# Performance work log

Measured on AMD Instinct MI355X. Metric: run time of the kernel, lower is better.

Reference implementation:

```python
import jax, jax.numpy as jnp
import numpy as np

B, N, L = 1, 2048, 256
DX, DY, H = 1536, 768, 12
D = DX // H  # head_dim = 128
EPS_MOD = 1e-6   # modulated_rmsnorm eps
EPS_QK = 1e-5    # per-head RMSNorm eps


def setup_inputs() -> dict:
    key = jax.random.key(0)
    ks = jax.random.split(key, 16)
    def n(k, shape, s=1.0):
        return jax.random.normal(k, shape, dtype=jnp.float32) * s
    # rotary tables: (N, H, D//2), shared across heads
    pos = jnp.arange(N, dtype=jnp.float32)
    inv_freq = 1.0 / (10000.0 ** (jnp.arange(D // 2, dtype=jnp.float32) / (D // 2)))
    ang = pos[:, None] * inv_freq[None, :]                       # (N, D/2)
    rope_cos = jnp.broadcast_to(jnp.cos(ang)[:, None, :], (N, H, D // 2))
    rope_sin = jnp.broadcast_to(jnp.sin(ang)[:, None, :], (N, H, D // 2))
    return {
        "x": n(ks[0], (B, N, DX)),
        "y": n(ks[1], (B, L, DY)),
        "scale_x": n(ks[2], (B, DX), 0.1),
        "scale_y": n(ks[3], (B, DY), 0.1),
        "rope_cos": rope_cos,
        "rope_sin": rope_sin,
        "Wqkv_x": n(ks[4], (DX, 3 * DX), 0.02),
        "bqkv_x": jnp.zeros((3 * DX,), jnp.float32),
        "Wqkv_y": n(ks[5], (DY, 3 * DX), 0.02),
        "bqkv_y": jnp.zeros((3 * DX,), jnp.float32),
        "q_norm_x_w": jnp.ones((D,), jnp.float32),
        "k_norm_x_w": jnp.ones((D,), jnp.float32),
        "q_norm_y_w": jnp.ones((D,), jnp.float32),
        "k_norm_y_w": jnp.ones((D,), jnp.float32),
        "Wproj_x": n(ks[6], (DX, DX), 0.02),
        "bproj_x": jnp.zeros((DX,), jnp.float32),
        "Wproj_y": n(ks[7], (DX, DY), 0.02),
        "bproj_y": jnp.zeros((DY,), jnp.float32),
    }


def _rms(v, eps):
    return v * jax.lax.rsqrt(jnp.mean(v * v, axis=-1, keepdims=True) + eps)


def _rope(q, cos, sin):
    # q: (B, S, H, D); cos/sin: (S, H, D/2); even/odd interleaved rotation
    qe, qo = q[..., 0::2], q[..., 1::2]
    re = qe * cos - qo * sin
    ro = qe * sin + qo * cos
    return jnp.stack([re, ro], axis=-1).reshape(q.shape)


def reference(x, y, scale_x, scale_y, rope_cos, rope_sin,
              Wqkv_x, bqkv_x, Wqkv_y, bqkv_y,
              q_norm_x_w, k_norm_x_w, q_norm_y_w, k_norm_y_w,
              Wproj_x, bproj_x, Wproj_y, bproj_y):
    b, n, dx = x.shape
    _, l, _ = y.shape
    h, d = H, D
    # --- visual stream ---
    xm = _rms(x, EPS_MOD) * (1.0 + scale_x[:, None, :])          # modulated_rmsnorm
    qkv = (xm @ Wqkv_x + bqkv_x).reshape(b, n, 3, h, d)
    q_x, k_x, v_x = qkv[:, :, 0], qkv[:, :, 1], qkv[:, :, 2]
    q_x = _rope(_rms(q_x, EPS_QK) * q_norm_x_w, rope_cos, rope_sin)
    k_x = _rope(_rms(k_x, EPS_QK) * k_norm_x_w, rope_cos, rope_sin)
    # --- text stream ---
    ym = _rms(y, EPS_MOD) * (1.0 + scale_y[:, None, :])
    qkvy = (ym @ Wqkv_y + bqkv_y).reshape(b, l, 3, h, d)
    q_y, k_y, v_y = qkvy[:, :, 0], qkvy[:, :, 1], qkvy[:, :, 2]
    q_y = _rms(q_y, EPS_QK) * q_norm_y_w
    k_y = _rms(k_y, EPS_QK) * k_norm_y_w
    # --- joint attention over concatenated sequence (B, H, N+L, D) ---
    q = jnp.concatenate([q_x, q_y], axis=1).transpose(0, 2, 1, 3)
    k = jnp.concatenate([k_x, k_y], axis=1).transpose(0, 2, 1, 3)
    v = jnp.concatenate([v_x, v_y], axis=1).transpose(0, 2, 1, 3)
    scale = 1.0 / np.sqrt(d).astype(np.float32)
    attn = jax.nn.softmax(jnp.einsum('bhqd,bhkd->bhqk', q, k) * scale, axis=-1)
    out = jnp.einsum('bhqk,bhkd->bhqd', attn, v)
    out = out.transpose(0, 2, 1, 3).reshape(b, n + l, h * d)
    x_out = out[:, :n] @ Wproj_x + bproj_x
    y_out = out[:, n:] @ Wproj_y + bproj_y
    return (x_out, y_out)
```

## Files before the change

kernel.cpp:

```cpp
#include <hip/hip_runtime.h>

typedef unsigned short u16;
typedef __attribute__((ext_vector_type(8))) short short8;
typedef __attribute__((ext_vector_type(4))) short short4v;
typedef __attribute__((ext_vector_type(4))) float floatx4;

__device__ __forceinline__ u16 f2bf(float f) {
  return (u16)((__float_as_uint(f) + 0x8000u) >> 16);
}
__device__ __forceinline__ float bf2f(u16 v) {
  return __uint_as_float(((unsigned)v) << 16);
}
__device__ __forceinline__ unsigned pack_bf2(float a, float b) {
  const unsigned ua = __float_as_uint(a) + 0x8000u;
  const unsigned ub = __float_as_uint(b) + 0x8000u;
  return __builtin_amdgcn_perm(ub, ua, 0x07060302);
}

#define GLD16(g, l) __builtin_amdgcn_global_load_lds( \
    (const __attribute__((address_space(1))) void*)(g), \
    (__attribute__((address_space(3))) void*)(l), 16, 0, 0)

__global__ __launch_bounds__(256) void prep(const float* __restrict__ W0, u16* __restrict__ T0,
                                            const float* __restrict__ W1, u16* __restrict__ T1,
                                            const float* __restrict__ W2, u16* __restrict__ T2,
                                            const float* __restrict__ W3, u16* __restrict__ T3,
                                            const float* __restrict__ x, const float* __restrict__ scale_x,
                                            const float* __restrict__ y, const float* __restrict__ scale_y,
                                            u16* __restrict__ xm, u16* __restrict__ ym) {
  __shared__ float t[32][33];
  const int z = blockIdx.z;
  if (z < 4) {
    const float* in; u16* out; int K, N;
    switch (z) {
      case 0: in = W0; out = T0; K = 1536; N = 4608; break;
      case 1: in = W1; out = T1; K = 768;  N = 4608; break;
      case 2: in = W2; out = T2; K = 1536; N = 1536; break;
      default: in = W3; out = T3; K = 1536; N = 768; break;
    }
    const int n0 = blockIdx.x * 32, k0 = blockIdx.y * 32;
    if (n0 >= N || k0 >= K) return;
    const int tx = threadIdx.x, ty = threadIdx.y;
#pragma unroll
    for (int i = 0; i < 32; i += 8)
      t[ty + i][tx] = in[(size_t)(k0 + ty + i) * N + n0 + tx];
    __syncthreads();
#pragma unroll
    for (int i = 0; i < 32; i += 8)
      out[(size_t)(n0 + ty + i) * K + k0 + tx] = f2bf(t[tx][ty + i]);
  } else {
    const int row = blockIdx.y * 144 + blockIdx.x;
    if (row >= 2304) return;
    const int tid = threadIdx.y * 32 + threadIdx.x;
    const float* xr; const float* sc; u16* dst; int D;
    if (row < 2048) { D = 1536; xr = x + (size_t)row * D; sc = scale_x; dst = xm + (size_t)row * D; }
    else { D = 768; xr = y + (size_t)(row - 2048) * D; sc = scale_y; dst = ym + (size_t)(row - 2048) * D; }
    float ss = 0.f;
    for (int c = tid; c < D; c += 256) { float v = xr[c]; ss += v * v; }
    for (int off = 32; off > 0; off >>= 1) ss += __shfl_down(ss, off);
    __shared__ float red[4];
    if ((tid & 63) == 0) red[tid >> 6] = ss;
    __syncthreads();
    const float tot = red[0] + red[1] + red[2] + red[3];
    const float r = rsqrtf(tot / (float)D + 1e-6f);
    for (int c = tid; c < D; c += 256)
      dst[c] = f2bf(xr[c] * r * (1.0f + sc[c]));
  }
}

template <bool BOUT>
__global__ __launch_bounds__(256) void gemm2(const u16* __restrict__ A0, const u16* __restrict__ BT0,
                                             const float* __restrict__ bias0, void* __restrict__ C0,
                                             int M0, int N0, int K0,
                                             const u16* __restrict__ A1, const u16* __restrict__ BT1,
                                             const float* __restrict__ bias1, void* __restrict__ C1,
                                             int M1, int N1, int K1) {
  const u16 *A, *BT; const float* bias; void* Cout; int M, N, K;
  if (blockIdx.z == 0) { A = A0; BT = BT0; bias = bias0; Cout = C0; M = M0; N = N0; K = K0; }
  else { A = A1; BT = BT1; bias = bias1; Cout = C1; M = M1; N = N1; K = K1; }
  const int bm = blockIdx.y * 128, bn = blockIdx.x * 128;
  if (bm >= M || bn >= N) return;

  __shared__ __align__(16) u16 As[128 * 32];
  __shared__ __align__(16) u16 Bs[128 * 32];
  const int tid = threadIdx.x;
  const int lane = tid & 63, wave = tid >> 6;
  const int wm = (wave & 1) * 64, wn = (wave >> 1) * 64;
  const int row16 = lane & 15, quad = lane >> 4;

  floatx4 acc[4][4] = {};
  const int r0 = lane >> 2, c4 = (lane & 3) * 8;
  const u16* Ag0 = A + (size_t)(bm + wave * 16 + r0) * K + c4;
  const u16* Ag1 = A + (size_t)(bm + (wave + 4) * 16 + r0) * K + c4;
  const u16* Bg0 = BT + (size_t)(bn + wave * 16 + r0) * K + c4;
  const u16* Bg1 = BT + (size_t)(bn + (wave + 4) * 16 + r0) * K + c4;
  u16* As0 = As + wave * 512; u16* As1 = As + (wave + 4) * 512;
  u16* Bs0 = Bs + wave * 512; u16* Bs1 = Bs + (wave + 4) * 512;

  for (int k0 = 0; k0 < K; k0 += 32) {
    GLD16(Ag0 + k0, As0);
    GLD16(Ag1 + k0, As1);
    GLD16(Bg0 + k0, Bs0);
    GLD16(Bg1 + k0, Bs1);
    __syncthreads();
    short8 af[4], bf[4];
#pragma unroll
    for (int i = 0; i < 4; i++) {
      af[i] = *(const short8*)&As[(wm + i * 16 + row16) * 32 + quad * 8];
      bf[i] = *(const short8*)&Bs[(wn + i * 16 + row16) * 32 + quad * 8];
    }
#pragma unroll
    for (int mi = 0; mi < 4; mi++)
#pragma unroll
      for (int ni = 0; ni < 4; ni++)
        acc[mi][ni] = __builtin_amdgcn_mfma_f32_16x16x32_bf16(af[mi], bf[ni], acc[mi][ni], 0, 0, 0);
    __syncthreads();
  }
#pragma unroll
  for (int mi = 0; mi < 4; mi++) {
#pragma unroll
    for (int ni = 0; ni < 4; ni++) {
      const int col = bn + wn + ni * 16 + row16;
      const float b = bias[col];
      const int row0 = bm + wm + mi * 16 + quad * 4;
#pragma unroll
      for (int r = 0; r < 4; r++) {
        const float v = acc[mi][ni][r] + b;
        if constexpr (BOUT)
          ((u16*)Cout)[(size_t)(row0 + r) * N + col] = f2bf(v);
        else
          ((float*)Cout)[(size_t)(row0 + r) * N + col] = v;
      }
    }
  }
}

__global__ __launch_bounds__(128) void qkv_post(const u16* __restrict__ qkvx,
                                                const u16* __restrict__ qkvy,
                                                const float* __restrict__ qnwx, const float* __restrict__ knwx,
                                                const float* __restrict__ qnwy, const float* __restrict__ knwy,
                                                const float* __restrict__ rcos, const float* __restrict__ rsin,
                                                u16* __restrict__ Q, u16* __restrict__ Kb, u16* __restrict__ V) {
  const int s = blockIdx.x, h = blockIdx.y, d = threadIdx.x;
  const bool isx = s < 2048;
  const u16* base = isx ? (qkvx + (size_t)s * 4608) : (qkvy + (size_t)(s - 2048) * 4608);
  const float q = bf2f(base[h * 128 + d]);
  const float k = bf2f(base[1536 + h * 128 + d]);
  const u16 v = base[3072 + h * 128 + d];
  __shared__ float redq[2], redk[2];
  float sq = q * q, sk = k * k;
  for (int off = 32; off > 0; off >>= 1) { sq += __shfl_down(sq, off); sk += __shfl_down(sk, off); }
  const int lane = threadIdx.x & 63, w = threadIdx.x >> 6;
  if (lane == 0) { redq[w] = sq; redk[w] = sk; }
  __syncthreads();
  const float rq = rsqrtf((redq[0] + redq[1]) * (1.f / 128.f) + 1e-5f);
  const float rk = rsqrtf((redk[0] + redk[1]) * (1.f / 128.f) + 1e-5f);
  float qn = q * rq * (isx ? qnwx[d] : qnwy[d]);
  float kn = k * rk * (isx ? knwx[d] : knwy[d]);
  if (isx) {
    const int i = d >> 1;
    const float c = rcos[((size_t)s * 12 + h) * 64 + i];
    const float sn = rsin[((size_t)s * 12 + h) * 64 + i];
    const float qo = __shfl_xor(qn, 1);
    const float ko = __shfl_xor(kn, 1);
    qn = (d & 1) ? (qo * sn + qn * c) : (qn * c - qo * sn);
    kn = (d & 1) ? (ko * sn + kn * c) : (kn * c - ko * sn);
  }
  qn *= 0.12751737942f;
  const size_t o = ((size_t)h * 2304 + s) * 128 + d;
  Q[o] = f2bf(qn);
  Kb[o] = f2bf(kn);
  V[o] = v;
}

__global__ __launch_bounds__(256) void vtrans(const u16* __restrict__ V, u16* __restrict__ Vt) {
  __shared__ u16 t[32][33];
  const int h = blockIdx.x, st = blockIdx.y * 32, dt = blockIdx.z * 32;
  const u16* Vh = V + (size_t)h * 2304 * 128;
  u16* Vth = Vt + (size_t)h * 128 * 2304;
  const int tx = threadIdx.x, ty = threadIdx.y;
#pragma unroll
  for (int i = 0; i < 32; i += 8)
    t[ty + i][tx] = Vh[(size_t)(st + ty + i) * 128 + dt + tx];
  __syncthreads();
#pragma unroll
  for (int i = 0; i < 32; i += 8)
    Vth[(size_t)(dt + ty + i) * 2304 + st + tx] = t[tx][ty + i];
}

__global__ __launch_bounds__(256, 4) void attn(const u16* __restrict__ Q, const u16* __restrict__ Kb,
                                               const u16* __restrict__ Vt,
                                               u16* __restrict__ Opart,
                                               float* __restrict__ Mp, float* __restrict__ Lp) {
  const int h = blockIdx.y, split = blockIdx.z;
  const int q0 = blockIdx.x * 64;
  const int tid = threadIdx.x, lane = tid & 63, wave = tid >> 6;
  const int row16 = lane & 15, quad = lane >> 4;
  const u16* Qh = Q + (size_t)h * 2304 * 128;
  const u16* Kh = Kb + (size_t)h * 2304 * 128;
  const u16* Vh = Vt + (size_t)h * 128 * 2304;

  __shared__ __align__(16) u16 Ks[64 * 128];
  __shared__ __align__(16) u16 Vs[128 * 64];
  __shared__ __align__(16) u16 Ps[4][16 * 64];

  short8 qf[4];
  {
    const u16* qrow = Qh + (size_t)(q0 + wave * 16 + row16) * 128;
#pragma unroll
    for (int kk = 0; kk < 4; kk++) qf[kk] = *(const short8*)(qrow + kk * 32 + quad * 8);
  }
  floatx4 oacc[8] = {};
  float m_i = -1e30f, l_i = 0.f;

  int krow[4], kcol[4], vrow[4], vcol[4];
#pragma unroll
  for (int i = 0; i < 4; i++) {
    const int j = i * 4 + wave;
    krow[i] = j * 4 + (lane >> 4);
    kcol[i] = ((lane & 15) ^ (krow[i] & 7)) * 8;
    vrow[i] = j * 8 + (lane >> 3);
    vcol[i] = ((lane & 7) ^ (vrow[i] & 7)) * 8;
  }
  const int sw = row16 & 7;
  const int kbeg = split * 576, kend = kbeg + 576;

  for (int kt = kbeg; kt < kend; kt += 64) {
    __syncthreads();
#pragma unroll
    for (int i = 0; i < 4; i++) {
      GLD16(Kh + (size_t)(kt + krow[i]) * 128 + kcol[i], Ks + (i * 4 + wave) * 512);
      GLD16(Vh + (size_t)vrow[i] * 2304 + kt + vcol[i], Vs + (i * 4 + wave) * 512);
    }
    __syncthreads();

    floatx4 sacc[4] = {};
#pragma unroll
    for (int mk = 0; mk < 4; mk++) {
#pragma unroll
      for (int kk = 0; kk < 4; kk++) {
        const int c = (4 * kk + quad) ^ sw;
        const short8 kfrag = *(const short8*)&Ks[(mk * 16 + row16) * 128 + c * 8];
        sacc[mk] = __builtin_amdgcn_mfma_f32_16x16x32_bf16(kfrag, qf[kk], sacc[mk], 0, 0, 0);
      }
    }
    float mx = sacc[0][0];
#pragma unroll
    for (int mk = 0; mk < 4; mk++)
#pragma unroll
      for (int r = 0; r < 4; r++) mx = fmaxf(mx, sacc[mk][r]);
    mx = fmaxf(mx, __shfl_xor(mx, 16));
    mx = fmaxf(mx, __shfl_xor(mx, 32));
    const float mnew = fmaxf(m_i, mx);
    if (__any(mnew > m_i)) {
      const float alpha = exp2f(m_i - mnew);
      m_i = mnew;
      const float a0 = __shfl(alpha, quad * 4 + 0);
      const float a1 = __shfl(alpha, quad * 4 + 1);
      const float a2 = __shfl(alpha, quad * 4 + 2);
      const float a3 = __shfl(alpha, quad * 4 + 3);
#pragma unroll
      for (int nd = 0; nd < 8; nd++) {
        oacc[nd][0] *= a0; oacc[nd][1] *= a1; oacc[nd][2] *= a2; oacc[nd][3] *= a3;
      }
      l_i *= alpha;
    }
    float s = 0.f;
#pragma unroll
    for (int mk = 0; mk < 4; mk++) {
#pragma unroll
      for (int r = 0; r < 4; r++) {
        const float p = exp2f(sacc[mk][r] - m_i);
        sacc[mk][r] = p;
        s += p;
      }
    }
    s += __shfl_xor(s, 16);
    s += __shfl_xor(s, 32);
    l_i += s;

#pragma unroll
    for (int mk = 0; mk < 4; mk++) {
      const int subp = (4 * mk + quad) ^ (sw << 1);
      uint2 pk;
      pk.x = pack_bf2(sacc[mk][0], sacc[mk][1]);
      pk.y = pack_bf2(sacc[mk][2], sacc[mk][3]);
      *(uint2*)&Ps[wave][row16 * 64 + subp * 4] = pk;
    }
    const int pc0 = quad ^ sw, pc1 = (4 + quad) ^ sw;
    const short8 pf0 = *(const short8*)&Ps[wave][row16 * 64 + pc0 * 8];
    const short8 pf1 = *(const short8*)&Ps[wave][row16 * 64 + pc1 * 8];
#pragma unroll
    for (int nd = 0; nd < 8; nd++) {
      const short8 vf0 = *(const short8*)&Vs[(nd * 16 + row16) * 64 + pc0 * 8];
      const short8 vf1 = *(const short8*)&Vs[(nd * 16 + row16) * 64 + pc1 * 8];
      oacc[nd] = __builtin_amdgcn_mfma_f32_16x16x32_bf16(pf0, vf0, oacc[nd], 0, 0, 0);
      oacc[nd] = __builtin_amdgcn_mfma_f32_16x16x32_bf16(pf1, vf1, oacc[nd], 0, 0, 0);
    }
  }
  const size_t base = (size_t)(split * 12 + h) * 2304 + q0 + wave * 16;
#pragma unroll
  for (int nd = 0; nd < 8; nd++)
#pragma unroll
    for (int r = 0; r < 4; r++)
      Opart[(base + quad * 4 + r) * 128 + nd * 16 + row16] = f2bf(oacc[nd][r]);
  if (lane < 16) { Mp[base + lane] = m_i; Lp[base + lane] = l_i; }
}

__global__ __launch_bounds__(256) void attn_combine(const u16* __restrict__ Opart,
                                                    const float* __restrict__ Mp,
                                                    const float* __restrict__ Lp,
                                                    u16* __restrict__ attnout) {
  const int idx = blockIdx.x * 256 + threadIdx.x;
  const int dd = (idx & 31) * 4;
  const int hq = idx >> 5;
  const int h = hq % 12, q = hq / 12;
  size_t b[4]; float ms[4], ls[4];
  float m = -1e30f;
#pragma unroll
  for (int s = 0; s < 4; s++) {
    b[s] = (size_t)(s * 12 + h) * 2304 + q;
    ms[s] = Mp[b[s]]; ls[s] = Lp[b[s]];
    m = fmaxf(m, ms[s]);
  }
  float w[4], denom = 0.f;
#pragma unroll
  for (int s = 0; s < 4; s++) { w[s] = exp2f(ms[s] - m); denom += ls[s] * w[s]; }
  const float inv = 1.0f / denom;
  float ox = 0.f, oy = 0.f, oz = 0.f, ow = 0.f;
#pragma unroll
  for (int s = 0; s < 4; s++) {
    const short4v o = *(const short4v*)&Opart[b[s] * 128 + dd];
    ox += bf2f((u16)o[0]) * w[s]; oy += bf2f((u16)o[1]) * w[s];
    oz += bf2f((u16)o[2]) * w[s]; ow += bf2f((u16)o[3]) * w[s];
  }
  short4v out;
  out[0] = (short)f2bf(ox * inv);
  out[1] = (short)f2bf(oy * inv);
  out[2] = (short)f2bf(oz * inv);
  out[3] = (short)f2bf(ow * inv);
  *(short4v*)&attnout[(size_t)idx * 4] = out;
}

extern "C" void kernel_launch(void* const* d_in, const int* in_sizes, int n_in,
                              void* d_out, int out_size, void* d_ws, size_t ws_size,
                              hipStream_t stream) {
  const float* x        = (const float*)d_in[0];
  const float* y        = (const float*)d_in[1];
  const float* scale_x  = (const float*)d_in[2];
  const float* scale_y  = (const float*)d_in[3];
  const float* rope_cos = (const float*)d_in[4];
  const float* rope_sin = (const float*)d_in[5];
  const float* Wqkv_x   = (const float*)d_in[6];
  const float* bqkv_x   = (const float*)d_in[7];
  const float* Wqkv_y   = (const float*)d_in[8];
  const float* bqkv_y   = (const float*)d_in[9];
  const float* qnwx     = (const float*)d_in[10];
  const float* knwx     = (const float*)d_in[11];
  const float* qnwy     = (const float*)d_in[12];
  const float* knwy     = (const float*)d_in[13];
  const float* Wproj_x  = (const float*)d_in[14];
  const float* bproj_x  = (const float*)d_in[15];
  const float* Wproj_y  = (const float*)d_in[16];
  const float* bproj_y  = (const float*)d_in[17];
  float* out = (float*)d_out;

  char* ws = (char*)d_ws;
  size_t off = 0;
  auto take = [&](size_t bytes) { char* p = ws + off; off += (bytes + 255) & ~(size_t)255; return p; };
  u16* WqkvxT  = (u16*)take((size_t)4608 * 1536 * 2);
  u16* WqkvyT  = (u16*)take((size_t)4608 * 768 * 2);
  u16* WprojxT = (u16*)take((size_t)1536 * 1536 * 2);
  u16* WprojyT = (u16*)take((size_t)768 * 1536 * 2);
  u16* xm      = (u16*)take((size_t)2048 * 1536 * 2);
  u16* ym      = (u16*)take((size_t)256 * 768 * 2);
  u16* qkvx    = (u16*)take((size_t)2048 * 4608 * 2);
  u16* qkvy    = (u16*)take((size_t)256 * 4608 * 2);
  u16* Qb      = (u16*)take((size_t)12 * 2304 * 128 * 2);
  u16* Kb      = (u16*)take((size_t)12 * 2304 * 128 * 2);
  u16* Vb      = (u16*)take((size_t)12 * 2304 * 128 * 2);
  u16* Vt      = (u16*)take((size_t)12 * 128 * 2304 * 2);
  u16* attnout = (u16*)take((size_t)2304 * 1536 * 2);
  u16* Opart   = (u16*)take((size_t)4 * 12 * 2304 * 128 * 2);
  float* Mp    = (float*)take((size_t)4 * 12 * 2304 * 4);
  float* Lp    = (float*)take((size_t)4 * 12 * 2304 * 4);

  prep<<<dim3(144, 48, 5), dim3(32, 8), 0, stream>>>(Wqkv_x, WqkvxT, Wqkv_y, WqkvyT,
                                                     Wproj_x, WprojxT, Wproj_y, WprojyT,
                                                     x, scale_x, y, scale_y, xm, ym);

  gemm2<true><<<dim3(36, 16, 2), 256, 0, stream>>>(xm, WqkvxT, bqkv_x, qkvx, 2048, 4608, 1536,
                                                   ym, WqkvyT, bqkv_y, qkvy, 256, 4608, 768);

  qkv_post<<<dim3(2304, 12), 128, 0, stream>>>(qkvx, qkvy, qnwx, knwx, qnwy, knwy,
                                               rope_cos, rope_sin, Qb, Kb, Vb);
  vtrans<<<dim3(12, 2304 / 32, 128 / 32), dim3(32, 8), 0, stream>>>(Vb, Vt);

  attn<<<dim3(2304 / 64, 12, 4), 256, 0, stream>>>(Qb, Kb, Vt, Opart, Mp, Lp);
  attn_combine<<<(2304 * 1536 / 4) / 256, 256, 0, stream>>>(Opart, Mp, Lp, attnout);

  gemm2<false><<<dim3(12, 16, 2), 256, 0, stream>>>(attnout, WprojxT, bproj_x, out, 2048, 1536, 1536,
                                                    attnout + (size_t)2048 * 1536, WprojyT, bproj_y,
                                                    out + (size_t)2048 * 1536, 256, 768, 1536);
  (void)in_sizes; (void)n_in; (void)out_size; (void)ws_size;
}
```

Measured before the change: 327.7 us.

## Fuse V transpose into qkv_post and double query rows per attention wave

qkv_post now handles 32 tokens per block with vectorized 16-element loads. It writes V directly in transposed layout through a shared-memory tile, so the separate vtrans kernel and the intermediate V buffer are gone. The attention kernel now processes 32 query rows per wave (128 per block), reusing each K/V LDS fragment for two MFMA groups, and switches to 6 KV splits with a vectorized 8-wide combine. The intent is to cut global traffic and K/V reloads per query, at the cost of higher register pressure (launch bounds lowered to 3 blocks per CU) and more partial outputs to combine.

```diff
diff --git a/kernel.cpp b/kernel.cpp
--- a/kernel.cpp
+++ b/kernel.cpp
@@ -135,65 +135,93 @@
   }
 }
 
-__global__ __launch_bounds__(128) void qkv_post(const u16* __restrict__ qkvx,
+__global__ __launch_bounds__(256) void qkv_post(const u16* __restrict__ qkvx,
                                                 const u16* __restrict__ qkvy,
                                                 const float* __restrict__ qnwx, const float* __restrict__ knwx,
                                                 const float* __restrict__ qnwy, const float* __restrict__ knwy,
                                                 const float* __restrict__ rcos, const float* __restrict__ rsin,
-                                                u16* __restrict__ Q, u16* __restrict__ Kb, u16* __restrict__ V) {
-  const int s = blockIdx.x, h = blockIdx.y, d = threadIdx.x;
-  const bool isx = s < 2048;
+                                                u16* __restrict__ Q, u16* __restrict__ Kb, u16* __restrict__ Vt) {
+  const int s0 = blockIdx.x * 32, h = blockIdx.y;
+  const int tid = threadIdx.x;
+  const int r = tid >> 3, j = tid & 7, d0 = j * 16;
+  const int s = s0 + r;
+  const bool isx = s0 < 2048;
   const u16* base = isx ? (qkvx + (size_t)s * 4608) : (qkvy + (size_t)(s - 2048) * 4608);
-  const float q = bf2f(base[h * 128 + d]);
-  const float k = bf2f(base[1536 + h * 128 + d]);
-  const u16 v = base[3072 + h * 128 + d];
-  __shared__ float redq[2], redk[2];
-  float sq = q * q, sk = k * k;
-  for (int off = 32; off > 0; off >>= 1) { sq += __shfl_down(sq, off); sk += __shfl_down(sk, off); }
-  const int lane = threadIdx.x & 63, w = threadIdx.x >> 6;
-  if (lane == 0) { redq[w] = sq; redk[w] = sk; }
+
+  __shared__ __align__(16) u16 Vtile[128][40];
+
+  short8 q8a = *(const short8*)(base + h * 128 + d0);
+  short8 q8b = *(const short8*)(base + h * 128 + d0 + 8);
+  short8 k8a = *(const short8*)(base + 1536 + h * 128 + d0);
+  short8 k8b = *(const short8*)(base + 1536 + h * 128 + d0 + 8);
+  short8 v8a = *(const short8*)(base + 3072 + h * 128 + d0);
+  short8 v8b = *(const short8*)(base + 3072 + h * 128 + d0 + 8);
+
+  float qv[16], kv[16];
+  float sq = 0.f, sk = 0.f;
+#pragma unroll
+  for (int i = 0; i < 8; i++) {
+    qv[i] = bf2f((u16)q8a[i]); qv[8 + i] = bf2f((u16)q8b[i]);
+    kv[i] = bf2f((u16)k8a[i]); kv[8 + i] = bf2f((u16)k8b[i]);
+  }
+#pragma unroll
+  for (int i = 0; i < 16; i++) { sq += qv[i] * qv[i]; sk += kv[i] * kv[i]; }
+  sq += __shfl_xor(sq, 1); sq += __shfl_xor(sq, 2); sq += __shfl_xor(sq, 4);
+  sk += __shfl_xor(sk, 1); sk += __shfl_xor(sk, 2); sk += __shfl_xor(sk, 4);
+  const float rq = rsqrtf(sq * (1.f / 128.f) + 1e-5f);
+  const float rk = rsqrtf(sk * (1.f / 128.f) + 1e-5f);
+
+  const float* qw = isx ? qnwx : qnwy;
+  const float* kw = isx ? knwx : knwy;
+#pragma unroll
+  for (int i = 0; i < 16; i++) {
+    qv[i] *= rq * qw[d0 + i];
+    kv[i] *= rk * kw[d0 + i];
+  }
+  if (isx) {
+    const float* cp = rcos + ((size_t)s * 12 + h) * 64 + d0 / 2;
+    const float* sp = rsin + ((size_t)s * 12 + h) * 64 + d0 / 2;
+#pragma unroll
+    for (int i = 0; i < 16; i += 2) {
+      const float c = cp[i / 2], sn = sp[i / 2];
+      const float qe = qv[i], qo = qv[i + 1];
+      const float ke = kv[i], ko = kv[i + 1];
+      qv[i] = qe * c - qo * sn; qv[i + 1] = qe * sn + qo * c;
+      kv[i] = ke * c - ko * sn; kv[i + 1] = ke * sn + ko * c;
+    }
+  }
+  short8 qo8[2], ko8[2];
+#pragma unroll
+  for (int half = 0; half < 2; half++)
+#pragma unroll
+    for (int i = 0; i < 8; i++) {
+      qo8[half][i] = (short)f2bf(qv[half * 8 + i] * 0.12751737942f);
+      ko8[half][i] = (short)f2bf(kv[half * 8 + i]);
+    }
+  const size_t o = ((size_t)h * 2304 + s) * 128 + d0;
+  *(short8*)(Q + o) = qo8[0];  *(short8*)(Q + o + 8) = qo8[1];
+  *(short8*)(Kb + o) = ko8[0]; *(short8*)(Kb + o + 8) = ko8[1];
+
+#pragma unroll
+  for (int i = 0; i < 8; i++) {
+    Vtile[d0 + i][r] = (u16)v8a[i];
+    Vtile[d0 + 8 + i][r] = (u16)v8b[i];
+  }
   __syncthreads();
-  const float rq = rsqrtf((redq[0] + redq[1]) * (1.f / 128.f) + 1e-5f);
-  const float rk = rsqrtf((redk[0] + redk[1]) * (1.f / 128.f) + 1e-5f);
-  float qn = q * rq * (isx ? qnwx[d] : qnwy[d]);
-  float kn = k * rk * (isx ? knwx[d] : knwy[d]);
-  if (isx) {
-    const int i = d >> 1;
-    const float c = rcos[((size_t)s * 12 + h) * 64 + i];
-    const float sn = rsin[((size_t)s * 12 + h) * 64 + i];
-    const float qo = __shfl_xor(qn, 1);
-    const float ko = __shfl_xor(kn, 1);
-    qn = (d & 1) ? (qo * sn + qn * c) : (qn * c - qo * sn);
-    kn = (d & 1) ? (ko * sn + kn * c) : (kn * c - ko * sn);
-  }
-  qn *= 0.12751737942f;
-  const size_t o = ((size_t)h * 2304 + s) * 128 + d;
-  Q[o] = f2bf(qn);
-  Kb[o] = f2bf(kn);
-  V[o] = v;
-}
-
-__global__ __launch_bounds__(256) void vtrans(const u16* __restrict__ V, u16* __restrict__ Vt) {
-  __shared__ u16 t[32][33];
-  const int h = blockIdx.x, st = blockIdx.y * 32, dt = blockIdx.z * 32;
-  const u16* Vh = V + (size_t)h * 2304 * 128;
-  u16* Vth = Vt + (size_t)h * 128 * 2304;
-  const int tx = threadIdx.x, ty = threadIdx.y;
-#pragma unroll
-  for (int i = 0; i < 32; i += 8)
-    t[ty + i][tx] = Vh[(size_t)(st + ty + i) * 128 + dt + tx];
-  __syncthreads();
-#pragma unroll
-  for (int i = 0; i < 32; i += 8)
-    Vth[(size_t)(dt + ty + i) * 2304 + st + tx] = t[tx][ty + i];
-}
-
-__global__ __launch_bounds__(256, 4) void attn(const u16* __restrict__ Q, const u16* __restrict__ Kb,
+  const int d = tid >> 1, sh = (tid & 1) * 16;
+  short8 va = *(const short8*)&Vtile[d][sh];
+  short8 vb = *(const short8*)&Vtile[d][sh + 8];
+  u16* vdst = Vt + ((size_t)h * 128 + d) * 2304 + s0 + sh;
+  *(short8*)vdst = va;
+  *(short8*)(vdst + 8) = vb;
+}
+
+__global__ __launch_bounds__(256, 3) void attn(const u16* __restrict__ Q, const u16* __restrict__ Kb,
                                                const u16* __restrict__ Vt,
                                                u16* __restrict__ Opart,
                                                float* __restrict__ Mp, float* __restrict__ Lp) {
   const int h = blockIdx.y, split = blockIdx.z;
-  const int q0 = blockIdx.x * 64;
+  const int q0 = blockIdx.x * 128;
   const int tid = threadIdx.x, lane = tid & 63, wave = tid >> 6;
   const int row16 = lane & 15, quad = lane >> 4;
   const u16* Qh = Q + (size_t)h * 2304 * 128;
@@ -202,28 +230,29 @@
 
   __shared__ __align__(16) u16 Ks[64 * 128];
   __shared__ __align__(16) u16 Vs[128 * 64];
-  __shared__ __align__(16) u16 Ps[4][16 * 64];
-
-  short8 qf[4];
-  {
-    const u16* qrow = Qh + (size_t)(q0 + wave * 16 + row16) * 128;
-#pragma unroll
-    for (int kk = 0; kk < 4; kk++) qf[kk] = *(const short8*)(qrow + kk * 32 + quad * 8);
-  }
-  floatx4 oacc[8] = {};
-  float m_i = -1e30f, l_i = 0.f;
+  __shared__ __align__(16) u16 Ps[4][32 * 64];
+
+  short8 qf[2][4];
+#pragma unroll
+  for (int g = 0; g < 2; g++) {
+    const u16* qrow = Qh + (size_t)(q0 + wave * 32 + g * 16 + row16) * 128;
+#pragma unroll
+    for (int kk = 0; kk < 4; kk++) qf[g][kk] = *(const short8*)(qrow + kk * 32 + quad * 8);
+  }
+  floatx4 oacc[8][2] = {};
+  float m_i[2] = {-1e30f, -1e30f}, l_i[2] = {0.f, 0.f};
 
   int krow[4], kcol[4], vrow[4], vcol[4];
 #pragma unroll
   for (int i = 0; i < 4; i++) {
-    const int j = i * 4 + wave;
-    krow[i] = j * 4 + (lane >> 4);
+    const int jj = i * 4 + wave;
+    krow[i] = jj * 4 + (lane >> 4);
     kcol[i] = ((lane & 15) ^ (krow[i] & 7)) * 8;
-    vrow[i] = j * 8 + (lane >> 3);
+    vrow[i] = jj * 8 + (lane >> 3);
     vcol[i] = ((lane & 7) ^ (vrow[i] & 7)) * 8;
   }
   const int sw = row16 & 7;
-  const int kbeg = split * 576, kend = kbeg + 576;
+  const int kbeg = split * 384, kend = kbeg + 384;
 
   for (int kt = kbeg; kt < kend; kt += 64) {
     __syncthreads();
@@ -234,77 +263,104 @@
     }
     __syncthreads();
 
-    floatx4 sacc[4] = {};
+    floatx4 sacc[4][2] = {};
 #pragma unroll
     for (int mk = 0; mk < 4; mk++) {
 #pragma unroll
       for (int kk = 0; kk < 4; kk++) {
         const int c = (4 * kk + quad) ^ sw;
         const short8 kfrag = *(const short8*)&Ks[(mk * 16 + row16) * 128 + c * 8];
-        sacc[mk] = __builtin_amdgcn_mfma_f32_16x16x32_bf16(kfrag, qf[kk], sacc[mk], 0, 0, 0);
-      }
-    }
-    float mx = sacc[0][0];
-#pragma unroll
-    for (int mk = 0; mk < 4; mk++)
-#pragma unroll
-      for (int r = 0; r < 4; r++) mx = fmaxf(mx, sacc[mk][r]);
-    mx = fmaxf(mx, __shfl_xor(mx, 16));
-    mx = fmaxf(mx, __shfl_xor(mx, 32));
-    const float mnew = fmaxf(m_i, mx);
-    if (__any(mnew > m_i)) {
-      const float alpha = exp2f(m_i - mnew);
-      m_i = mnew;
-      const float a0 = __shfl(alpha, quad * 4 + 0);
-      const float a1 = __shfl(alpha, quad * 4 + 1);
-      const float a2 = __shfl(alpha, quad * 4 + 2);
-      const float a3 = __shfl(alpha, quad * 4 + 3);
-#pragma unroll
-      for (int nd = 0; nd < 8; nd++) {
-        oacc[nd][0] *= a0; oacc[nd][1] *= a1; oacc[nd][2] *= a2; oacc[nd][3] *= a3;
-      }
-      l_i *= alpha;
-    }
-    float s = 0.f;
-#pragma unroll
-    for (int mk = 0; mk < 4; mk++) {
+        sacc[mk][0] = __builtin_amdgcn_mfma_f32_16x16x32_bf16(kfrag, qf[0][kk], sacc[mk][0], 0, 0, 0);
+        sacc[mk][1] = __builtin_amdgcn_mfma_f32_16x16x32_bf16(kfrag, qf[1][kk], sacc[mk][1], 0, 0, 0);
+      }
+    }
+    float mnew[2];
+#pragma unroll
+    for (int g = 0; g < 2; g++) {
+      float mx = sacc[0][g][0];
+#pragma unroll
+      for (int mk = 0; mk < 4; mk++)
+#pragma unroll
+        for (int r = 0; r < 4; r++) mx = fmaxf(mx, sacc[mk][g][r]);
+      mx = fmaxf(mx, __shfl_xor(mx, 16));
+      mx = fmaxf(mx, __shfl_xor(mx, 32));
+      mnew[g] = fmaxf(m_i[g], mx);
+    }
+    if (__any(mnew[0] > m_i[0] || mnew[1] > m_i[1])) {
+      const float al0 = exp2f(m_i[0] - mnew[0]);
+      const float al1 = exp2f(m_i[1] - mnew[1]);
+      m_i[0] = mnew[0]; m_i[1] = mnew[1];
+      float a[4][2];
 #pragma unroll
       for (int r = 0; r < 4; r++) {
-        const float p = exp2f(sacc[mk][r] - m_i);
-        sacc[mk][r] = p;
-        s += p;
-      }
-    }
-    s += __shfl_xor(s, 16);
-    s += __shfl_xor(s, 32);
-    l_i += s;
-
-#pragma unroll
-    for (int mk = 0; mk < 4; mk++) {
-      const int subp = (4 * mk + quad) ^ (sw << 1);
-      uint2 pk;
-      pk.x = pack_bf2(sacc[mk][0], sacc[mk][1]);
-      pk.y = pack_bf2(sacc[mk][2], sacc[mk][3]);
-      *(uint2*)&Ps[wave][row16 * 64 + subp * 4] = pk;
-    }
+        a[r][0] = __shfl(al0, quad * 4 + r);
+        a[r][1] = __shfl(al1, quad * 4 + r);
+      }
+#pragma unroll
+      for (int nd = 0; nd < 8; nd++)
+#pragma unroll
+        for (int g = 0; g < 2; g++) {
+          oacc[nd][g][0] *= a[0][g]; oacc[nd][g][1] *= a[1][g];
+          oacc[nd][g][2] *= a[2][g]; oacc[nd][g][3] *= a[3][g];
+        }
+      l_i[0] *= al0; l_i[1] *= al1;
+    }
+#pragma unroll
+    for (int g = 0; g < 2; g++) {
+      float s = 0.f;
+#pragma unroll
+      for (int mk = 0; mk < 4; mk++) {
+#pragma unroll
+        for (int r = 0; r < 4; r++) {
+          const float p = exp2f(sacc[mk][g][r] - m_i[g]);
+          sacc[mk][g][r] = p;
+          s += p;
+        }
+      }
+      s += __shfl_xor(s, 16);
+      s += __shfl_xor(s, 32);
+      l_i[g] += s;
+    }
+#pragma unroll
+    for (int g = 0; g < 2; g++)
+#pragma unroll
+      for (int mk = 0; mk < 4; mk++) {
+        const int subp = (4 * mk + quad) ^ (sw << 1);
+        uint2 pk;
+        pk.x = pack_bf2(sacc[mk][g][0], sacc[mk][g][1]);
+        pk.y = pack_bf2(sacc[mk][g][2], sacc[mk][g][3]);
+        *(uint2*)&Ps[wave][(g * 16 + row16) * 64 + subp * 4] = pk;
+      }
     const int pc0 = quad ^ sw, pc1 = (4 + quad) ^ sw;
-    const short8 pf0 = *(const short8*)&Ps[wave][row16 * 64 + pc0 * 8];
-    const short8 pf1 = *(const short8*)&Ps[wave][row16 * 64 + pc1 * 8];
+    short8 pf[2][2];
+#pragma unroll
+    for (int g = 0; g < 2; g++) {
+      pf[g][0] = *(const short8*)&Ps[wave][(g * 16 + row16) * 64 + pc0 * 8];
+      pf[g][1] = *(const short8*)&Ps[wave][(g * 16 + row16) * 64 + pc1 * 8];
+    }
 #pragma unroll
     for (int nd = 0; nd < 8; nd++) {
       const short8 vf0 = *(const short8*)&Vs[(nd * 16 + row16) * 64 + pc0 * 8];
       const short8 vf1 = *(const short8*)&Vs[(nd * 16 + row16) * 64 + pc1 * 8];
-      oacc[nd] = __builtin_amdgcn_mfma_f32_16x16x32_bf16(pf0, vf0, oacc[nd], 0, 0, 0);
-      oacc[nd] = __builtin_amdgcn_mfma_f32_16x16x32_bf16(pf1, vf1, oacc[nd], 0, 0, 0);
-    }
-  }
-  const size_t base = (size_t)(split * 12 + h) * 2304 + q0 + wave * 16;
+#pragma unroll
+      for (int g = 0; g < 2; g++) {
+        oacc[nd][g] = __builtin_amdgcn_mfma_f32_16x16x32_bf16(pf[g][0], vf0, oacc[nd][g], 0, 0, 0);
+        oacc[nd][g] = __builtin_amdgcn_mfma_f32_16x16x32_bf16(pf[g][1], vf1, oacc[nd][g], 0, 0, 0);
+      }
+    }
+  }
+  const size_t base = (size_t)(split * 12 + h) * 2304 + q0 + wave * 32;
 #pragma unroll
   for (int nd = 0; nd < 8; nd++)
 #pragma unroll
-    for (int r = 0; r < 4; r++)
-      Opart[(base + quad * 4 + r) * 128 + nd * 16 + row16] = f2bf(oacc[nd][r]);
-  if (lane < 16) { Mp[base + lane] = m_i; Lp[base + lane] = l_i; }
+    for (int g = 0; g < 2; g++)
+#pragma unroll
+      for (int r = 0; r < 4; r++)
+        Opart[(base + g * 16 + quad * 4 + r) * 128 + nd * 16 + row16] = f2bf(oacc[nd][g][r]);
+  if (lane < 16) {
+    Mp[base + lane] = m_i[0];      Lp[base + lane] = l_i[0];
+    Mp[base + 16 + lane] = m_i[1]; Lp[base + 16 + lane] = l_i[1];
+  }
 }
 
 __global__ __launch_bounds__(256) void attn_combine(const u16* __restrict__ Opart,
@@ -312,34 +368,32 @@
                                                     const float* __restrict__ Lp,
                                                     u16* __restrict__ attnout) {
   const int idx = blockIdx.x * 256 + threadIdx.x;
-  const int dd = (idx & 31) * 4;
-  const int hq = idx >> 5;
+  const int dd = (idx & 15) * 8;
+  const int hq = idx >> 4;
   const int h = hq % 12, q = hq / 12;
-  size_t b[4]; float ms[4], ls[4];
+  size_t b[6]; float ms[6], ls[6];
   float m = -1e30f;
 #pragma unroll
-  for (int s = 0; s < 4; s++) {
+  for (int s = 0; s < 6; s++) {
     b[s] = (size_t)(s * 12 + h) * 2304 + q;
     ms[s] = Mp[b[s]]; ls[s] = Lp[b[s]];
     m = fmaxf(m, ms[s]);
   }
-  float w[4], denom = 0.f;
-#pragma unroll
-  for (int s = 0; s < 4; s++) { w[s] = exp2f(ms[s] - m); denom += ls[s] * w[s]; }
+  float w[6], denom = 0.f;
+#pragma unroll
+  for (int s = 0; s < 6; s++) { w[s] = exp2f(ms[s] - m); denom += ls[s] * w[s]; }
   const float inv = 1.0f / denom;
-  float ox = 0.f, oy = 0.f, oz = 0.f, ow = 0.f;
-#pragma unroll
-  for (int s = 0; s < 4; s++) {
-    const short4v o = *(const short4v*)&Opart[b[s] * 128 + dd];
-    ox += bf2f((u16)o[0]) * w[s]; oy += bf2f((u16)o[1]) * w[s];
-    oz += bf2f((u16)o[2]) * w[s]; ow += bf2f((u16)o[3]) * w[s];
-  }
-  short4v out;
-  out[0] = (short)f2bf(ox * inv);
-  out[1] = (short)f2bf(oy * inv);
-  out[2] = (short)f2bf(oz * inv);
-  out[3] = (short)f2bf(ow * inv);
-  *(short4v*)&attnout[(size_t)idx * 4] = out;
+  float acc[8] = {};
+#pragma unroll
+  for (int s = 0; s < 6; s++) {
+    const short8 o = *(const short8*)&Opart[b[s] * 128 + dd];
+#pragma unroll
+    for (int i = 0; i < 8; i++) acc[i] += bf2f((u16)o[i]) * w[s];
+  }
+  short8 outv;
+#pragma unroll
+  for (int i = 0; i < 8; i++) outv[i] = (short)f2bf(acc[i] * inv);
+  *(short8*)&attnout[(size_t)idx * 8] = outv;
 }
 
 extern "C" void kernel_launch(void* const* d_in, const int* in_sizes, int n_in,
@@ -378,12 +432,11 @@
   u16* qkvy    = (u16*)take((size_t)256 * 4608 * 2);
   u16* Qb      = (u16*)take((size_t)12 * 2304 * 128 * 2);
   u16* Kb      = (u16*)take((size_t)12 * 2304 * 128 * 2);
-  u16* Vb      = (u16*)take((size_t)12 * 2304 * 128 * 2);
   u16* Vt      = (u16*)take((size_t)12 * 128 * 2304 * 2);
   u16* attnout = (u16*)take((size_t)2304 * 1536 * 2);
-  u16* Opart   = (u16*)take((size_t)4 * 12 * 2304 * 128 * 2);
-  float* Mp    = (float*)take((size_t)4 * 12 * 2304 * 4);
-  float* Lp    = (float*)take((size_t)4 * 12 * 2304 * 4);
+  u16* Opart   = (u16*)take((size_t)6 * 12 * 2304 * 128 * 2);
+  float* Mp    = (float*)take((size_t)6 * 12 * 2304 * 4);
+  float* Lp    = (float*)take((size_t)6 * 12 * 2304 * 4);
 
   prep<<<dim3(144, 48, 5), dim3(32, 8), 0, stream>>>(Wqkv_x, WqkvxT, Wqkv_y, WqkvyT,
                                                      Wproj_x, WprojxT, Wproj_y, WprojyT,
@@ -392,12 +445,11 @@
   gemm2<true><<<dim3(36, 16, 2), 256, 0, stream>>>(xm, WqkvxT, bqkv_x, qkvx, 2048, 4608, 1536,
                                                    ym, WqkvyT, bqkv_y, qkvy, 256, 4608, 768);
 
-  qkv_post<<<dim3(2304, 12), 128, 0, stream>>>(qkvx, qkvy, qnwx, knwx, qnwy, knwy,
-                                               rope_cos, rope_sin, Qb, Kb, Vb);
-  vtrans<<<dim3(12, 2304 / 32, 128 / 32), dim3(32, 8), 0, stream>>>(Vb, Vt);
-
-  attn<<<dim3(2304 / 64, 12, 4), 256, 0, stream>>>(Qb, Kb, Vt, Opart, Mp, Lp);
-  attn_combine<<<(2304 * 1536 / 4) / 256, 256, 0, stream>>>(Opart, Mp, Lp, attnout);
+  qkv_post<<<dim3(72, 12), 256, 0, stream>>>(qkvx, qkvy, qnwx, knwx, qnwy, knwy,
+                                             rope_cos, rope_sin, Qb, Kb, Vt);
+
+  attn<<<dim3(2304 / 128, 12, 6), 256, 0, stream>>>(Qb, Kb, Vt, Opart, Mp, Lp);
+  attn_combine<<<(2304 * 1536 / 8) / 256, 256, 0, stream>>>(Opart, Mp, Lp, attnout);
 
   gemm2<false><<<dim3(12, 16, 2), 256, 0, stream>>>(attnout, WprojxT, bproj_x, out, 2048, 1536, 1536,
                                                     attnout + (size_t)2048 * 1536, WprojyT, bproj_y,
```

Measured after the change: 345.4 us. +5.4%, slower.
